# Optimization experiments

Hardware: AMD Instinct MI355X
Metric: run time of the kernel (lower is better)

Reference implementation:

```python
import jax, jax.numpy as jnp
import numpy as np

N, E = 50000, 500000
DH, DL = 13, 128          # handcrafted / learned node feature dims
OH, OL = 32, 96           # node-encoder output dims; node_dim D = OH+OL
D = OH + OL               # 128
EIN = (DH + DL) + 1 + 3 * D + 1  # 527, forced by concat in forward
H = 256                   # MLP hidden width
HC = 64                   # classifier hidden width
EPS = 1e-8


def _mlp(x, W1, b1, W2, b2):
    # 2-layer MLP with ReLU, matching repo MLP(fc_dims=[H, out])
    return jax.nn.relu(x @ W1 + b1) @ W2 + b2


def _cosine(a, b):
    # torch.nn.CosineSimilarity(dim=1, eps=1e-8)
    na = jnp.maximum(jnp.linalg.norm(a, axis=-1), EPS)
    nb = jnp.maximum(jnp.linalg.norm(b, axis=-1), EPS)
    return jnp.sum(a * b, axis=-1) / (na * nb)


def _lin(key, fan_in, fan_out):
    kW, kb = jax.random.split(key)
    s = 1.0 / np.sqrt(fan_in)
    return (jax.random.uniform(kW, (fan_in, fan_out), jnp.float32, -s, s),
            jax.random.uniform(kb, (fan_out,), jnp.float32, -s, s))


def setup_inputs() -> dict:
    key = jax.random.key(0)
    ks = jax.random.split(key, 16)
    x1 = jax.random.normal(ks[0], (N, DH), jnp.float32)
    x2 = jax.random.normal(ks[1], (N, DL), jnp.float32)
    edge_index = jax.random.randint(ks[2], (2, E), 0, N, jnp.int64)
    Wh1, bh1 = _lin(ks[3], DH, H);   Wh2, bh2 = _lin(ks[4], H, OH)
    Wl1, bl1 = _lin(ks[5], DL, H);   Wl2, bl2 = _lin(ks[6], H, OL)
    We1, be1 = _lin(ks[7], EIN, H);  We2, be2 = _lin(ks[8], H, D)
    Wmsg, bmsg = _lin(ks[9], 2 * D, D)
    Wnode, bnode = _lin(ks[10], 2 * D, D)
    Wmp1, bmp1 = _lin(ks[11], 3 * D, H); Wmp2, bmp2 = _lin(ks[12], H, D)
    Wc1, bc1 = _lin(ks[13], D, HC);  Wc2, bc2 = _lin(ks[14], HC, 1)
    return dict(x1=x1, x2=x2, edge_index=edge_index,
                Wh1=Wh1, bh1=bh1, Wh2=Wh2, bh2=bh2,
                Wl1=Wl1, bl1=bl1, Wl2=Wl2, bl2=bl2,
                We1=We1, be1=be1, We2=We2, be2=be2,
                Wmsg=Wmsg, bmsg=bmsg, Wnode=Wnode, bnode=bnode,
                Wmp1=Wmp1, bmp1=bmp1, Wmp2=Wmp2, bmp2=bmp2,
                Wc1=Wc1, bc1=bc1, Wc2=Wc2, bc2=bc2)


def reference(x1, x2, edge_index,
              Wh1, bh1, Wh2, bh2,
              Wl1, bl1, Wl2, bl2,
              We1, be1, We2, be2,
              Wmsg, bmsg, Wnode, bnode,
              Wmp1, bmp1, Wmp2, bmp2,
              Wc1, bc1, Wc2, bc2):
    src, trg = edge_index[0], edge_index[1]
    # raw-feature edge descriptors
    x_init = jnp.concatenate((x1, x2), axis=-1)            # [N, 141]
    xi_s, xi_t = x_init[src], x_init[trg]                  # gathers [E, 141]
    sim1 = _cosine(xi_s, xi_t)                             # [E]
    abs_init = jnp.abs(xi_s - xi_t)                        # [E, 141]
    # node encoders
    h1 = _mlp(x1, Wh1, bh1, Wh2, bh2)                      # [N, 32]
    h2 = _mlp(x2, Wl1, bl1, Wl2, bl2)                      # [N, 96]
    x = jnp.concatenate((h1, h2), axis=-1)                 # [N, 128]
    xs, xt = x[src], x[trg]                                # [E, 128]
    sim2 = _cosine(xs, xt)                                 # [E]
    edge_feat_in = jnp.concatenate(
        (abs_init, sim1[:, None], xs, xt, jnp.abs(xs - xt), sim2[:, None]),
        axis=-1)                                           # [E, 527]
    e = _mlp(edge_feat_in, We1, be1, We2, be2)             # [E, 128]
    # edge MPNN round: edge->node aggregation, node update, edge update
    msg = jax.nn.relu(jnp.concatenate((xs, e), axis=-1) @ Wmsg + bmsg)  # [E, 128]
    agg = jax.ops.segment_sum(msg, trg, num_segments=N)    # [N, 128]
    xn = jax.nn.relu(jnp.concatenate((x, agg), axis=-1) @ Wnode + bnode)  # [N, 128]
    e_mp = _mlp(jnp.concatenate((xn[src], xn[trg], e), axis=-1),
                Wmp1, bmp1, Wmp2, bmp2)                    # [E, 128]
    pred = _mlp(e_mp, Wc1, bc1, Wc2, bc2)                  # [E, 1]
    return jnp.squeeze(pred, axis=-1)                      # [E]
```

## Files before the change

### kernel.cpp

```cpp
#include <hip/hip_runtime.h>
#include <hip/hip_bf16.h>
#include <hip/hip_fp16.h>


using fp16 = __half;
typedef _Float16 h16;
typedef _Float16 f16x8 __attribute__((ext_vector_type(8)));
typedef _Float16 h16x2 __attribute__((ext_vector_type(2)));
typedef short s16x8 __attribute__((ext_vector_type(8)));
typedef float f32x4 __attribute__((ext_vector_type(4)));

#define NN 50000
#define EE 500000
#define EPSC 1e-8f
#define SCAN_B 196

__device__ __forceinline__ float reluf(float v){ return v > 0.f ? v : 0.f; }

__device__ __forceinline__ float dot8(const f16x8 a, const f16x8 b, float acc)
{
#pragma unroll
  for (int i = 0; i < 4; ++i) {
    const h16x2 av = {a[2 * i], a[2 * i + 1]};
    const h16x2 bv = {b[2 * i], b[2 * i + 1]};
    acc = __builtin_amdgcn_fdot2(av, bv, acc, false);
  }
  return acc;
}

__device__ __forceinline__ f16x8 absdiff8(const f16x8 a, const f16x8 b)
{
  const f16x8 d = a - b;
  s16x8 di = __builtin_bit_cast(s16x8, d);
  di &= (short)0x7fff;
  return __builtin_bit_cast(f16x8, di);
}

#define OFF_E1   0
#define OFF_E2   139264
#define OFF_MSG  172032
#define OFF_NODE 204800
#define OFF_MP1  237568
#define OFF_MP2  335872
#define OFF_C1   368640
#define OFF_N1   376832
#define OFF_N2   458752
#define WT_TOTAL 524288
#define BF_TOTAL 640

__global__ __launch_bounds__(256) void k_prep(
    const float* __restrict__ We1, const float* __restrict__ We2,
    const float* __restrict__ Wmsg, const float* __restrict__ Wnode,
    const float* __restrict__ Wmp1, const float* __restrict__ Wmp2,
    const float* __restrict__ Wc1,
    const float* __restrict__ Wh1, const float* __restrict__ Wl1,
    const float* __restrict__ Wh2, const float* __restrict__ Wl2,
    const float* __restrict__ bh1, const float* __restrict__ bl1,
    const float* __restrict__ bh2, const float* __restrict__ bl2,
    h16* __restrict__ WT, float* __restrict__ BF)
{
  int idx = blockIdx.x * 256 + threadIdx.x;
  if (idx >= WT_TOTAL) {
    const int b = idx - WT_TOTAL;
    if (b < 512) BF[b] = (b < 256) ? bh1[b] : bl1[b - 256];
    else if (b < BF_TOTAL) {
      const int c = b - 512;
      BF[b] = (c < 32) ? bh2[c] : bl2[c - 32];
    }
    return;
  }
  h16 v;
  if (idx < OFF_E2) {
    const int L = idx, n = L / 544, k = L % 544;
    int r;
    if      (k < 128) r = 142 + k;
    else if (k < 256) r = 270 + (k - 128);
    else if (k < 384) r = 398 + (k - 256);
    else if (k < 512) r = 13 + (k - 384);
    else if (k < 525) r = k - 512;
    else if (k == 528) r = 141;
    else if (k == 529) r = 526;
    else r = -1;
    v = (h16)((r >= 0) ? We1[r * 256 + n] : 0.f);
  } else if (idx < OFF_MSG) {
    const int L = idx - OFF_E2, n = L >> 8, k = L & 255;
    v = (h16)We2[k * 128 + n];
  } else if (idx < OFF_NODE) {
    const int L = idx - OFF_MSG, n = L >> 8, k = L & 255;
    const int ko = (k < 128) ? (128 + k) : (k - 128);
    v = (h16)Wmsg[ko * 128 + n];
  } else if (idx < OFF_MP1) {
    const int L = idx - OFF_NODE, n = L >> 8, k = L & 255;
    v = (h16)Wnode[k * 128 + n];
  } else if (idx < OFF_MP2) {
    const int L = idx - OFF_MP1, n = L / 384, k = L % 384;
    v = (h16)Wmp1[k * 256 + n];
  } else if (idx < OFF_C1) {
    const int L = idx - OFF_MP2, n = L >> 8, k = L & 255;
    v = (h16)Wmp2[k * 128 + n];
  } else if (idx < OFF_N1) {
    const int L = idx - OFF_C1, n = L >> 7, k = L & 127;
    v = (h16)Wc1[k * 64 + n];
  } else if (idx < OFF_N2) {
    const int L = idx - OFF_N1, n = L / 160, k = L % 160;
    float f = 0.f;
    if (n < 256) { if (k < 13) f = Wh1[k * 256 + n]; }
    else { if (k >= 16 && k < 144) f = Wl1[(k - 16) * 256 + (n - 256)]; }
    v = (h16)f;
  } else {
    const int L = idx - OFF_N2, n = L >> 9, k = L & 511;
    float f = 0.f;
    if (n < 32) { if (k < 256) f = Wh2[k * 32 + n]; }
    else { if (k >= 256) f = Wl2[(k - 256) * 96 + (n - 32)]; }
    v = (h16)f;
  }
  WT[idx] = v;
}

__global__ __launch_bounds__(256) void k_cvt(
    const float* __restrict__ x1, const float* __restrict__ x2,
    const int* __restrict__ ei,
    h16* __restrict__ X1P, h16* __restrict__ X2H, int* __restrict__ CNT)
{
  const int idx = blockIdx.x * 256 + threadIdx.x;
  if (idx < EE) atomicAdd(&CNT[ei[EE + idx]], 1);
  if (idx < NN * 16) {
    const int nn = idx >> 4, j = idx & 15;
    X1P[idx] = (h16)((j < 13) ? x1[nn * 13 + j] : 0.f);
  }
  const int i2 = idx - NN * 16;
  if (i2 >= 0 && i2 < NN * 128) X2H[i2] = (h16)x2[i2];
}

__global__ __launch_bounds__(256) void k_scanA(
    const int* __restrict__ CNT, int* __restrict__ TEX, int* __restrict__ BS)
{
  __shared__ int sd[256];
  const int tid = threadIdx.x;
  const int i = blockIdx.x * 256 + tid;
  const int v = (i < NN) ? CNT[i] : 0;
  sd[tid] = v;
  __syncthreads();
  for (int off = 1; off < 256; off <<= 1) {
    const int x = (tid >= off) ? sd[tid - off] : 0;
    __syncthreads();
    sd[tid] += x;
    __syncthreads();
  }
  if (i < NN) TEX[i] = sd[tid] - v;
  if (tid == 255) BS[blockIdx.x] = sd[255];
}

__global__ __launch_bounds__(256) void k_scanB(
    const int* __restrict__ BS, int* __restrict__ BSSE)
{
  __shared__ int sd[256];
  const int tid = threadIdx.x;
  const int v = (tid < SCAN_B) ? BS[tid] : 0;
  sd[tid] = v;
  __syncthreads();
  for (int off = 1; off < 256; off <<= 1) {
    const int x = (tid >= off) ? sd[tid - off] : 0;
    __syncthreads();
    sd[tid] += x;
    __syncthreads();
  }
  if (tid < SCAN_B) BSSE[tid] = sd[tid] - v;
}

__global__ __launch_bounds__(256) void k_scatter(
    const int* __restrict__ ei, const int* __restrict__ TEX,
    const int* __restrict__ BSSE, int* __restrict__ POS,
    int* __restrict__ ES, int* __restrict__ ET, int* __restrict__ OID)
{
  const int e = blockIdx.x * 256 + threadIdx.x;
  if (e >= EE) return;
  const int t = ei[EE + e];
  const int p = atomicAdd(&POS[t], 1);
  const int idx = BSSE[t >> 8] + TEX[t] + p;
  ES[idx] = ei[e];
  ET[idx] = t;
  OID[idx] = e;
}

template<int ROWS, int UDIM, int KP, int LDA, int WAVES, bool RELU,
         bool ENDSYNC, typename F>
__device__ __forceinline__ void mfma_gemm(const h16* sA,
    const h16* __restrict__ WT, const float* __restrict__ bias, F emit)
{
  constexpr int RT = ROWS / 16;
  constexpr int NPW0 = UDIM / WAVES;
  constexpr int NPW = (NPW0 < 16) ? 16 : NPW0;
  constexpr int NT = NPW / 16;
  constexpr int NSTEPS = KP / 32;
  constexpr int CH0 = (NT >= 4) ? 2 : 4;
  constexpr int CHUNK = (NSTEPS < CH0) ? NSTEPS : CH0;
  constexpr int NCH = (NSTEPS + CHUNK - 1) / CHUNK;
  const int tid = threadIdx.x;
  const int wave = tid >> 6;
  const int lane = tid & 63;
  const int m = lane & 15;
  const int quad = lane >> 4;
  const int n0 = wave * NPW;
  const bool active = (n0 < UDIM);

  f32x4 acc[RT][NT];
#pragma unroll
  for (int r = 0; r < RT; ++r)
#pragma unroll
    for (int j = 0; j < NT; ++j) acc[r][j] = (f32x4){0.f, 0.f, 0.f, 0.f};
  float bb[NT];

  if (active) {
    const h16* wbase = &WT[(size_t)(n0 + m) * KP + quad * 8];
#pragma unroll
    for (int j = 0; j < NT; ++j) bb[j] = bias[n0 + j * 16 + m];

    f16x8 breg[2][CHUNK][NT];
#pragma unroll
    for (int s = 0; s < CHUNK; ++s)
      if (s < NSTEPS)
#pragma unroll
        for (int j = 0; j < NT; ++j)
          breg[0][s][j] = *(const f16x8*)&wbase[(size_t)j * 16 * KP + s * 32];
    asm volatile("" ::: "memory");

#pragma unroll
    for (int c = 0; c < NCH; ++c) {
      if (c + 1 < NCH) {
#pragma unroll
        for (int s = 0; s < CHUNK; ++s) {
          const int st = (c + 1) * CHUNK + s;
          if (st < NSTEPS)
#pragma unroll
            for (int j = 0; j < NT; ++j)
              breg[(c + 1) & 1][s][j] =
                  *(const f16x8*)&wbase[(size_t)j * 16 * KP + st * 32];
        }
      }
#pragma unroll
      for (int s = 0; s < CHUNK; ++s) {
        const int st = c * CHUNK + s;
        if (st < NSTEPS) {
          const int k0 = st * 32;
#pragma unroll
          for (int r = 0; r < RT; ++r) {
            const f16x8 af = *(const f16x8*)&sA[(r * 16 + m) * LDA + k0 + quad * 8];
#pragma unroll
            for (int j = 0; j < NT; ++j)
              acc[r][j] = __builtin_amdgcn_mfma_f32_16x16x32_f16(af, breg[c & 1][s][j], acc[r][j], 0, 0, 0);
          }
        }
      }
      asm volatile("" ::: "memory");
    }
  }
  __syncthreads();
  if (active) {
#pragma unroll
    for (int j = 0; j < NT; ++j) {
      const int col = n0 + j * 16 + m;
#pragma unroll
      for (int r = 0; r < RT; ++r)
#pragma unroll
        for (int g = 0; g < 4; ++g) {
          const int row = r * 16 + quad * 4 + g;
          float v = acc[r][j][g] + bb[j];
          if (RELU) v = reluf(v);
          emit(row, col, v);
        }
    }
  }
  if (ENDSYNC) __syncthreads();
}

__global__ __launch_bounds__(512, 4) void k_nenc(
    const h16* __restrict__ X1P, const h16* __restrict__ X2H,
    const h16* __restrict__ WT, const float* __restrict__ BF,
    h16* __restrict__ XH)
{
  __shared__ __align__(16) h16 sA[32 * 168];
  __shared__ __align__(16) h16 sH[32 * 520];
  const int tid = threadIdx.x;
  const int n0 = blockIdx.x * 32;
  const int remn = NN - n0;
  const int cnt = remn < 32 ? remn : 32;
  const int n = tid >> 4;
  const int q = tid & 15;

  if (n < cnt) {
    const int node = n0 + n;
    if (q < 2)
      *(f16x8*)&sA[n * 168 + q * 8] = *(const f16x8*)&X1P[node * 16 + q * 8];
    else if (q < 4)
      *(f16x8*)&sA[n * 168 + 144 + (q - 2) * 8] = (f16x8){};
    *(f16x8*)&sA[n * 168 + 16 + q * 8] =
        *(const f16x8*)&X2H[(size_t)node * 128 + q * 8];
  }
  __syncthreads();

  mfma_gemm<32, 512, 160, 168, 8, true, true>(sA, WT + OFF_N1, BF,
      [&](int row, int col, float v) { sH[row * 520 + col] = (h16)v; });
  mfma_gemm<32, 128, 512, 520, 8, false, false>(sH, WT + OFF_N2, BF + 512,
      [&](int row, int col, float v) {
        if (row < cnt) XH[(size_t)(n0 + row) * 128 + col] = (h16)v;
      });
}

__global__ __launch_bounds__(512, 4) void k_edge_mlp(
    const h16* __restrict__ X1P, const h16* __restrict__ X2H,
    const int* __restrict__ ES, const int* __restrict__ ET,
    const h16* __restrict__ XH, const h16* __restrict__ WT,
    const float* __restrict__ be1, const float* __restrict__ be2,
    const float* __restrict__ bmsg,
    h16* __restrict__ EB, float* __restrict__ AGG)
{
  __shared__ __align__(16) h16 sFeat[64 * 568];
  __shared__ int strg[64];
  const int tid = threadIdx.x;
  const long e0 = (long)blockIdx.x * 64;
  const long rem = (long)EE - e0;
  const int cnt = rem < 64 ? (int)rem : 64;
  const int n = tid >> 3;
  const int q = tid & 7;
  h16* Arow = &sFeat[n * 568];
  f16x8 xsv0 = {}, xsv1 = {};

  if (n < cnt) {
    const int s = ES[e0 + n];
    const int t = ET[e0 + n];
    if (q == 0) strg[n] = t;
    float ds = 0.f, ns = 0.f, nt = 0.f;
    if (q < 2) {
      const f16x8 a = *(const f16x8*)&X1P[s * 16 + q * 8];
      const f16x8 b = *(const f16x8*)&X1P[t * 16 + q * 8];
      ds = dot8(a, b, ds); ns = dot8(a, a, ns); nt = dot8(b, b, nt);
      *(f16x8*)&Arow[512 + q * 8] = absdiff8(a, b);
    }
#pragma unroll
    for (int c = 0; c < 2; ++c) {
      const f16x8 a = *(const f16x8*)&X2H[(size_t)s * 128 + q * 16 + c * 8];
      const f16x8 b = *(const f16x8*)&X2H[(size_t)t * 128 + q * 16 + c * 8];
      ds = dot8(a, b, ds); ns = dot8(a, a, ns); nt = dot8(b, b, nt);
      *(f16x8*)&Arow[384 + q * 16 + c * 8] = absdiff8(a, b);
    }
    ds += __shfl_xor(ds, 1); ds += __shfl_xor(ds, 2); ds += __shfl_xor(ds, 4);
    ns += __shfl_xor(ns, 1); ns += __shfl_xor(ns, 2); ns += __shfl_xor(ns, 4);
    nt += __shfl_xor(nt, 1); nt += __shfl_xor(nt, 2); nt += __shfl_xor(nt, 4);
    if (q == 0)
      Arow[528] = (h16)(ds / (fmaxf(sqrtf(ns), EPSC) * fmaxf(sqrtf(nt), EPSC)));

    float ds2 = 0.f, ns2 = 0.f, nt2 = 0.f;
#pragma unroll
    for (int c = 0; c < 2; ++c) {
      const f16x8 a = *(const f16x8*)&XH[(size_t)s * 128 + q * 16 + c * 8];
      const f16x8 b = *(const f16x8*)&XH[(size_t)t * 128 + q * 16 + c * 8];
      if (c == 0) xsv0 = a; else xsv1 = a;
      ds2 = dot8(a, b, ds2); ns2 = dot8(a, a, ns2); nt2 = dot8(b, b, nt2);
      *(f16x8*)&Arow[q * 16 + c * 8]       = a;
      *(f16x8*)&Arow[128 + q * 16 + c * 8] = b;
      *(f16x8*)&Arow[256 + q * 16 + c * 8] = absdiff8(a, b);
    }
    ds2 += __shfl_xor(ds2, 1); ds2 += __shfl_xor(ds2, 2); ds2 += __shfl_xor(ds2, 4);
    ns2 += __shfl_xor(ns2, 1); ns2 += __shfl_xor(ns2, 2); ns2 += __shfl_xor(ns2, 4);
    nt2 += __shfl_xor(nt2, 1); nt2 += __shfl_xor(nt2, 2); nt2 += __shfl_xor(nt2, 4);
    if (q == 0)
      Arow[529] = (h16)(ds2 / (fmaxf(sqrtf(ns2), EPSC) * fmaxf(sqrtf(nt2), EPSC)));
    for (int j = 530 + q; j < 544; j += 8) Arow[j] = (h16)0.f;
  } else {
    if (q == 0) strg[n] = 0;
    for (int j8 = q; j8 < 71; j8 += 8) *(f16x8*)&Arow[j8 * 8] = (f16x8){};
  }
  __syncthreads();

  h16* sHid = sFeat;
  mfma_gemm<64, 256, 544, 568, 8, true, true>(sFeat, WT + OFF_E1, be1,
      [&](int row, int col, float v) { sHid[row * 264 + col] = (h16)v; });
  mfma_gemm<64, 128, 256, 264, 8, false, false>(sHid, WT + OFF_E2, be2,
      [&](int row, int col, float v) {
        const h16 vh = (h16)v;
        if (row < cnt) EB[(size_t)(e0 + row) * 128 + col] = vh;
        sHid[row * 264 + col] = vh;
      });
  *(f16x8*)&sFeat[n * 264 + 128 + q * 16]     = xsv0;
  *(f16x8*)&sFeat[n * 264 + 128 + q * 16 + 8] = xsv1;
  __syncthreads();
  mfma_gemm<64, 128, 256, 264, 8, true, true>(sFeat, WT + OFF_MSG, bmsg,
      [&](int row, int col, float v) {
        *(float*)((char*)sFeat + row * 528 + col * 4) = v;
      });
  {
    const int c = tid & 127;
    const int g = tid >> 7;
    const int r0 = g * 16;
    if (r0 < cnt) {
      const int rend = (r0 + 16 < cnt) ? r0 + 16 : cnt;
      float acc = 0.f;
      int cur = strg[r0];
      for (int r = r0; r < rend; ++r) {
        const int t = strg[r];
        if (t != cur) {
          atomicAdd(&AGG[(size_t)cur * 128 + c], acc);
          acc = 0.f; cur = t;
        }
        acc += *(const float*)((const char*)sFeat + r * 528 + c * 4);
      }
      atomicAdd(&AGG[(size_t)cur * 128 + c], acc);
    }
  }
}

__global__ __launch_bounds__(256, 4) void k_node_update(
    const h16* __restrict__ XH, const float* __restrict__ AGG,
    const h16* __restrict__ WT, const float* __restrict__ bnode,
    h16* __restrict__ XNH)
{
  __shared__ __align__(16) h16 sA[64 * 264];
  const int tid = threadIdx.x;
  const int n0 = blockIdx.x * 64;
  const int remn = NN - n0;
  const int cnt = remn < 64 ? remn : 64;
  const int n = tid >> 2;
  const int q = tid & 3;

  if (n < cnt) {
    const f16x8* xr = (const f16x8*)&XH[(size_t)(n0 + n) * 128];
    const float4* ar = (const float4*)&AGG[(size_t)(n0 + n) * 128];
    for (int j8 = q; j8 < 16; j8 += 4)
      *(f16x8*)&sA[n * 264 + j8 * 8] = xr[j8];
    for (int j4 = q; j4 < 32; j4 += 4) {
      const float4 b = ar[j4];
      h16* p1 = &sA[n * 264 + 128 + j4 * 4];
      p1[0] = (h16)b.x; p1[1] = (h16)b.y; p1[2] = (h16)b.z; p1[3] = (h16)b.w;
    }
  } else {
    for (int j = q; j < 256; j += 4) sA[n * 264 + j] = (h16)0.f;
  }
  __syncthreads();

  mfma_gemm<64, 128, 256, 264, 4, true, false>(sA, WT + OFF_NODE, bnode,
      [&](int row, int col, float v) {
        if (row < cnt) XNH[(size_t)(n0 + row) * 128 + col] = (h16)v;
      });
}

__global__ __launch_bounds__(512, 4) void k_empl(
    const int* __restrict__ ES, const int* __restrict__ ET,
    const int* __restrict__ OID, const h16* __restrict__ XNH,
    const h16* __restrict__ EB, const h16* __restrict__ WT,
    const float* __restrict__ bmp1, const float* __restrict__ bmp2,
    const float* __restrict__ bc1,
    const float* __restrict__ Wc2, const float* __restrict__ bc2,
    float* __restrict__ out)
{
  __shared__ __align__(16) h16 sF[64 * 392];
  const int tid = threadIdx.x;
  const long e0 = (long)blockIdx.x * 64;
  const long rem = (long)EE - e0;
  const int cnt = rem < 64 ? (int)rem : 64;
  const int n = tid >> 3;
  const int q = tid & 7;

  if (n < cnt) {
    const int s = ES[e0 + n];
    const int t = ET[e0 + n];
    const f16x8* xsr = (const f16x8*)&XNH[(size_t)s * 128];
    const f16x8* xtr = (const f16x8*)&XNH[(size_t)t * 128];
    const f16x8* ebr = (const f16x8*)&EB[(size_t)(e0 + n) * 128];
#pragma unroll
    for (int j8 = q; j8 < 16; j8 += 8) {
      *(f16x8*)&sF[n * 392 + j8 * 8]       = xsr[j8];
      *(f16x8*)&sF[n * 392 + 128 + j8 * 8] = xtr[j8];
      *(f16x8*)&sF[n * 392 + 256 + j8 * 8] = ebr[j8];
    }
  } else {
    for (int j8 = q; j8 < 49; j8 += 8) *(f16x8*)&sF[n * 392 + j8 * 8] = (f16x8){};
  }
  __syncthreads();

  h16*  sH2 = sF;
  h16*  sE  = sF;
  float* sHC = (float*)((char*)sF + 17408);
  mfma_gemm<64, 256, 384, 392, 8, true, true>(sF, WT + OFF_MP1, bmp1,
      [&](int row, int col, float v) { sH2[row * 264 + col] = (h16)v; });
  mfma_gemm<64, 128, 256, 264, 8, false, true>(sH2, WT + OFF_MP2, bmp2,
      [&](int row, int col, float v) { sE[row * 136 + col] = (h16)v; });
  mfma_gemm<64, 64, 128, 136, 8, true, true>(sE, WT + OFF_C1, bc1,
      [&](int row, int col, float v) { sHC[row * 65 + col] = v; });
  if (tid < cnt) {
    float acc = bc2[0];
    for (int k = 0; k < 64; ++k) acc += sHC[tid * 65 + k] * Wc2[k];
    out[OID[e0 + tid]] = acc;
  }
}

extern "C" void kernel_launch(void* const* d_in, const int* in_sizes, int n_in,
                              void* d_out, int out_size, void* d_ws, size_t ws_size,
                              hipStream_t stream)
{
  const float* x1  = (const float*)d_in[0];
  const float* x2  = (const float*)d_in[1];
  const int*   ei  = (const int*)d_in[2];
  const float* Wh1 = (const float*)d_in[3],  *bh1 = (const float*)d_in[4];
  const float* Wh2 = (const float*)d_in[5],  *bh2 = (const float*)d_in[6];
  const float* Wl1 = (const float*)d_in[7],  *bl1 = (const float*)d_in[8];
  const float* Wl2 = (const float*)d_in[9],  *bl2 = (const float*)d_in[10];
  const float* We1 = (const float*)d_in[11], *be1 = (const float*)d_in[12];
  const float* We2 = (const float*)d_in[13], *be2 = (const float*)d_in[14];
  const float* Wmsg = (const float*)d_in[15], *bmsg = (const float*)d_in[16];
  const float* Wnode = (const float*)d_in[17], *bnode = (const float*)d_in[18];
  const float* Wmp1 = (const float*)d_in[19], *bmp1 = (const float*)d_in[20];
  const float* Wmp2 = (const float*)d_in[21], *bmp2 = (const float*)d_in[22];
  const float* Wc1 = (const float*)d_in[23], *bc1 = (const float*)d_in[24];
  const float* Wc2 = (const float*)d_in[25], *bc2 = (const float*)d_in[26];
  float* out = (float*)d_out;

  float* AGG = (float*)d_ws;
  h16*   EB  = (h16*)(AGG + (size_t)NN * 128);
  h16*   WT  = EB + (size_t)EE * 128;
  h16*   XH  = WT + WT_TOTAL;
  h16*   XNH = XH + (size_t)NN * 128;
  h16*   X1P = XNH + (size_t)NN * 128;
  h16*   X2H = X1P + (size_t)NN * 16;
  float* BF  = (float*)(X2H + (size_t)NN * 128);
  int*   CNT = (int*)(BF + BF_TOTAL);
  int*   POS = CNT + NN;
  int*   TEX = POS + NN;
  int*   ES  = TEX + NN;
  int*   ET  = ES + EE;
  int*   OID = ET + EE;
  int*   BS  = OID + EE;
  int*   BSSE = BS + 256;

  k_prep<<<(WT_TOTAL + BF_TOTAL + 255) / 256, 256, 0, stream>>>(
      We1, We2, Wmsg, Wnode, Wmp1, Wmp2, Wc1,
      Wh1, Wl1, Wh2, Wl2, bh1, bl1, bh2, bl2, WT, BF);
  hipMemsetAsync(AGG, 0, (size_t)NN * 128 * sizeof(float), stream);
  hipMemsetAsync(CNT, 0, (size_t)2 * NN * sizeof(int), stream);
  k_cvt<<<(NN * 16 + NN * 128 + 255) / 256, 256, 0, stream>>>(
      x1, x2, ei, X1P, X2H, CNT);
  k_scanA<<<SCAN_B, 256, 0, stream>>>(CNT, TEX, BS);
  k_scanB<<<1, 256, 0, stream>>>(BS, BSSE);
  k_scatter<<<(EE + 255) / 256, 256, 0, stream>>>(ei, TEX, BSSE, POS, ES, ET, OID);
  k_nenc<<<(NN + 31) / 32, 512, 0, stream>>>(X1P, X2H, WT, BF, XH);
  k_edge_mlp<<<7813, 512, 0, stream>>>(X1P, X2H, ES, ET, XH, WT,
                                       be1, be2, bmsg, EB, AGG);
  k_node_update<<<782, 256, 0, stream>>>(XH, AGG, WT, bnode, XNH);
  k_empl<<<7813, 512, 0, stream>>>(ES, ET, OID, XNH, EB, WT, bmp1, bmp2, bc1,
                                   Wc2, bc2, out);
}
```

Baseline: 867.4 us.

## Split GEMM waves across row groups as well as columns

Generalizes the shared MFMA GEMM helper so the block's waves form a 2D grid of row groups times column groups, instead of every wave covering all rows and a thin column slice. Each GEMM call gets a row-split factor, and the weight prefetch chunk shrinks when a wave holds many column tiles. The goal is fewer redundant LDS reads of the activation tile and keeping all waves busy on narrow outputs such as the 64-wide classifier layer. The cost is that each weight column is now fetched by several waves, which raises global/L2 weight traffic and per-wave register use.

```diff
diff --git a/kernel.cpp b/kernel.cpp
--- a/kernel.cpp
+++ b/kernel.cpp
@@ -183,17 +183,19 @@
   OID[idx] = e;
 }
 
-template<int ROWS, int UDIM, int KP, int LDA, int WAVES, bool RELU,
+template<int ROWS, int UDIM, int KP, int LDA, int WAVES, int RS, bool RELU,
          bool ENDSYNC, typename F>
 __device__ __forceinline__ void mfma_gemm(const h16* sA,
     const h16* __restrict__ WT, const float* __restrict__ bias, F emit)
 {
-  constexpr int RT = ROWS / 16;
-  constexpr int NPW0 = UDIM / WAVES;
+  constexpr int CS = WAVES / RS;
+  constexpr int RG = ROWS / RS;
+  constexpr int RT = RG / 16;
+  constexpr int NPW0 = UDIM / CS;
   constexpr int NPW = (NPW0 < 16) ? 16 : NPW0;
   constexpr int NT = NPW / 16;
   constexpr int NSTEPS = KP / 32;
-  constexpr int CH0 = (NT >= 4) ? 2 : 4;
+  constexpr int CH0 = (NT >= 8) ? 1 : ((NT >= 4) ? 2 : 4);
   constexpr int CHUNK = (NSTEPS < CH0) ? NSTEPS : CH0;
   constexpr int NCH = (NSTEPS + CHUNK - 1) / CHUNK;
   const int tid = threadIdx.x;
@@ -201,7 +203,10 @@
   const int lane = tid & 63;
   const int m = lane & 15;
   const int quad = lane >> 4;
-  const int n0 = wave * NPW;
+  const int wr = wave % RS;
+  const int wc = wave / RS;
+  const int rbase = wr * RG;
+  const int n0 = wc * NPW;
   const bool active = (n0 < UDIM);
 
   f32x4 acc[RT][NT];
@@ -245,7 +250,7 @@
           const int k0 = st * 32;
 #pragma unroll
           for (int r = 0; r < RT; ++r) {
-            const f16x8 af = *(const f16x8*)&sA[(r * 16 + m) * LDA + k0 + quad * 8];
+            const f16x8 af = *(const f16x8*)&sA[(rbase + r * 16 + m) * LDA + k0 + quad * 8];
 #pragma unroll
             for (int j = 0; j < NT; ++j)
               acc[r][j] = __builtin_amdgcn_mfma_f32_16x16x32_f16(af, breg[c & 1][s][j], acc[r][j], 0, 0, 0);
@@ -264,7 +269,7 @@
       for (int r = 0; r < RT; ++r)
 #pragma unroll
         for (int g = 0; g < 4; ++g) {
-          const int row = r * 16 + quad * 4 + g;
+          const int row = rbase + r * 16 + quad * 4 + g;
           float v = acc[r][j][g] + bb[j];
           if (RELU) v = reluf(v);
           emit(row, col, v);
@@ -299,9 +304,9 @@
   }
   __syncthreads();
 
-  mfma_gemm<32, 512, 160, 168, 8, true, true>(sA, WT + OFF_N1, BF,
+  mfma_gemm<32, 512, 160, 168, 8, 2, true, true>(sA, WT + OFF_N1, BF,
       [&](int row, int col, float v) { sH[row * 520 + col] = (h16)v; });
-  mfma_gemm<32, 128, 512, 520, 8, false, false>(sH, WT + OFF_N2, BF + 512,
+  mfma_gemm<32, 128, 512, 520, 8, 2, false, false>(sH, WT + OFF_N2, BF + 512,
       [&](int row, int col, float v) {
         if (row < cnt) XH[(size_t)(n0 + row) * 128 + col] = (h16)v;
       });
@@ -374,9 +379,9 @@
   __syncthreads();
 
   h16* sHid = sFeat;
-  mfma_gemm<64, 256, 544, 568, 8, true, true>(sFeat, WT + OFF_E1, be1,
+  mfma_gemm<64, 256, 544, 568, 8, 2, true, true>(sFeat, WT + OFF_E1, be1,
       [&](int row, int col, float v) { sHid[row * 264 + col] = (h16)v; });
-  mfma_gemm<64, 128, 256, 264, 8, false, false>(sHid, WT + OFF_E2, be2,
+  mfma_gemm<64, 128, 256, 264, 8, 4, false, false>(sHid, WT + OFF_E2, be2,
       [&](int row, int col, float v) {
         const h16 vh = (h16)v;
         if (row < cnt) EB[(size_t)(e0 + row) * 128 + col] = vh;
@@ -385,7 +390,7 @@
   *(f16x8*)&sFeat[n * 264 + 128 + q * 16]     = xsv0;
   *(f16x8*)&sFeat[n * 264 + 128 + q * 16 + 8] = xsv1;
   __syncthreads();
-  mfma_gemm<64, 128, 256, 264, 8, true, true>(sFeat, WT + OFF_MSG, bmsg,
+  mfma_gemm<64, 128, 256, 264, 8, 4, true, true>(sFeat, WT + OFF_MSG, bmsg,
       [&](int row, int col, float v) {
         *(float*)((char*)sFeat + row * 528 + col * 4) = v;
       });
@@ -438,7 +443,7 @@
   }
   __syncthreads();
 
-  mfma_gemm<64, 128, 256, 264, 4, true, false>(sA, WT + OFF_NODE, bnode,
+  mfma_gemm<64, 128, 256, 264, 4, 2, true, false>(sA, WT + OFF_NODE, bnode,
       [&](int row, int col, float v) {
         if (row < cnt) XNH[(size_t)(n0 + row) * 128 + col] = (h16)v;
       });
@@ -481,11 +486,11 @@
   h16*  sH2 = sF;
   h16*  sE  = sF;
   float* sHC = (float*)((char*)sF + 17408);
-  mfma_gemm<64, 256, 384, 392, 8, true, true>(sF, WT + OFF_MP1, bmp1,
+  mfma_gemm<64, 256, 384, 392, 8, 2, true, true>(sF, WT + OFF_MP1, bmp1,
       [&](int row, int col, float v) { sH2[row * 264 + col] = (h16)v; });
-  mfma_gemm<64, 128, 256, 264, 8, false, true>(sH2, WT + OFF_MP2, bmp2,
+  mfma_gemm<64, 128, 256, 264, 8, 4, false, true>(sH2, WT + OFF_MP2, bmp2,
       [&](int row, int col, float v) { sE[row * 136 + col] = (h16)v; });
-  mfma_gemm<64, 64, 128, 136, 8, true, true>(sE, WT + OFF_C1, bc1,
+  mfma_gemm<64, 64, 128, 136, 8, 4, true, true>(sE, WT + OFF_C1, bc1,
       [&](int row, int col, float v) { sHC[row * 65 + col] = v; });
   if (tid < cnt) {
     float acc = bc2[0];
```

Result: slower. 1.682 ms (+94.0%).
